# Performance work log

Hardware: AMD Instinct MI355X
Metric: run time of the kernel (lower is better)

Reference implementation:

```python
import jax, jax.numpy as jnp
import numpy as np

N, E = 50000, 600000
D_IN, D_H, D_OUT, D_E = 128, 128, 128, 32


def setup_inputs() -> dict:
    key = jax.random.key(0)
    ks = jax.random.split(key, 20)
    s = 0.05
    inp = {
        "x": jax.random.normal(ks[0], (N, D_IN), dtype=jnp.float32),
        "edge_index": jax.random.randint(ks[1], (2, E), 0, N, dtype=jnp.int64),
        "edge_attr": jax.random.normal(ks[2], (E, D_E), dtype=jnp.float32),
        # layer 0 (GINEConv MLP + edge lin: edge_dim -> in_channels)
        "w1_0": jax.random.normal(ks[3], (D_IN, D_H), dtype=jnp.float32) * s,
        "b1_0": jnp.zeros((D_H,), jnp.float32),
        "w2_0": jax.random.normal(ks[4], (D_H, D_H), dtype=jnp.float32) * s,
        "b2_0": jnp.zeros((D_H,), jnp.float32),
        "we_0": jax.random.normal(ks[5], (D_E, D_IN), dtype=jnp.float32) * s,
        "be_0": jnp.zeros((D_IN,), jnp.float32),
        # layer 1 (edge lin: edge_dim -> hidden_channels)
        "w1_1": jax.random.normal(ks[6], (D_H, D_H), dtype=jnp.float32) * s,
        "b1_1": jnp.zeros((D_H,), jnp.float32),
        "w2_1": jax.random.normal(ks[7], (D_H, D_H), dtype=jnp.float32) * s,
        "b2_1": jnp.zeros((D_H,), jnp.float32),
        "we_1": jax.random.normal(ks[8], (D_E, D_H), dtype=jnp.float32) * s,
        "be_1": jnp.zeros((D_H,), jnp.float32),
        # output head
        "fc1_w": jax.random.normal(ks[9], (D_H, D_H), dtype=jnp.float32) * s,
        "fc1_b": jnp.zeros((D_H,), jnp.float32),
        "fc2_w": jax.random.normal(ks[10], (D_H, D_OUT), dtype=jnp.float32) * s,
        "fc2_b": jnp.zeros((D_OUT,), jnp.float32),
    }
    return inp


def _gine_layer(x, src, dst, edge_attr, we, be, w1, b1, w2, b2):
    # GINEConv (eps=0): out = MLP(x + sum_j ReLU(x_j + edge_lin(e_ij)))
    e_emb = edge_attr @ we + be                       # [E, d]
    msg = jax.nn.relu(x[src] + e_emb)                 # gather + message
    agg = jax.ops.segment_sum(msg, dst, num_segments=x.shape[0])  # scatter-add
    h = agg + x                                       # (1 + eps) * x, eps = 0
    return jnp.maximum(h @ w1 + b1, 0.0) @ w2 + b2    # 2-layer MLP


def reference(x, edge_index, edge_attr,
              w1_0, b1_0, w2_0, b2_0, we_0, be_0,
              w1_1, b1_1, w2_1, b2_1, we_1, be_1,
              fc1_w, fc1_b, fc2_w, fc2_b):
    src, dst = edge_index[0], edge_index[1]
    h = _gine_layer(x, src, dst, edge_attr, we_0, be_0, w1_0, b1_0, w2_0, b2_0)
    h = jax.nn.relu(h)  # activation (dropout=0 -> identity)
    h = _gine_layer(h, src, dst, edge_attr, we_1, be_1, w1_1, b1_1, w2_1, b2_1)
    h = jax.nn.relu(h)
    h = jax.nn.relu(h @ fc1_w + fc1_b)
    return h @ fc2_w + fc2_b
```

## Files before the change

kernel.cpp:

```cpp
#include <hip/hip_runtime.h>
#include <stdint.h>


#define ND 128
#define ED 32

typedef __attribute__((ext_vector_type(8))) short short8;
typedef __attribute__((ext_vector_type(4))) float f32x4;

__device__ inline unsigned short bf16_hi(float f) {
    union { float f; unsigned u; } v;
    v.f = f;
    return (unsigned short)(v.u >> 16);
}
__device__ inline float bf16_f(unsigned short h) {
    union { unsigned u; float f; } v;
    v.u = ((unsigned)h) << 16;
    return v.f;
}

__global__ __launch_bounds__(256) void zero_kernel(int* __restrict__ p, int n) {
    int i = blockIdx.x * blockDim.x + threadIdx.x;
    if (i < n) p[i] = 0;
}

__global__ __launch_bounds__(256) void hist_kernel(const int* __restrict__ ei,
                                                   int* __restrict__ counts, int E) {
    int i = blockIdx.x * blockDim.x + threadIdx.x;
    if (i < E) atomicAdd(&counts[ei[E + i]], 1);
}

__global__ __launch_bounds__(256) void bsum_kernel(const int* __restrict__ counts,
                                                   int* __restrict__ bsum, int N) {
    __shared__ int s[256];
    int t = threadIdx.x;
    int i = blockIdx.x * 256 + t;
    s[t] = (i < N) ? counts[i] : 0;
    __syncthreads();
#pragma unroll
    for (int off = 128; off > 0; off >>= 1) {
        if (t < off) s[t] += s[t + off];
        __syncthreads();
    }
    if (t == 0) bsum[blockIdx.x] = s[0];
}

__global__ __launch_bounds__(256) void scan_bsums(const int* __restrict__ bsum,
                                                  int* __restrict__ bofs,
                                                  int* __restrict__ row_start_N, int NB) {
    __shared__ int s[256];
    int t = threadIdx.x;
    int chunk = (NB + 255) >> 8;
    int lo = min(t * chunk, NB);
    int hi = min(lo + chunk, NB);
    int sum = 0;
    for (int i = lo; i < hi; ++i) sum += bsum[i];
    s[t] = sum;
    __syncthreads();
    for (int off = 1; off < 256; off <<= 1) {
        int v = (t >= off) ? s[t - off] : 0;
        __syncthreads();
        s[t] += v;
        __syncthreads();
    }
    int pre = (t == 0) ? 0 : s[t - 1];
    for (int i = lo; i < hi; ++i) {
        bofs[i] = pre;
        pre += bsum[i];
    }
    if (t == 255) *row_start_N = s[255];
}

__global__ __launch_bounds__(256) void expand_kernel(const int* __restrict__ counts,
                                                     const int* __restrict__ bofs,
                                                     int* __restrict__ row_start,
                                                     int* __restrict__ woff, int N) {
    __shared__ int s[256];
    int t = threadIdx.x;
    int i = blockIdx.x * 256 + t;
    int c = (i < N) ? counts[i] : 0;
    s[t] = c;
    __syncthreads();
    for (int off = 1; off < 256; off <<= 1) {
        int v = (t >= off) ? s[t - off] : 0;
        __syncthreads();
        s[t] += v;
        __syncthreads();
    }
    if (i < N) {
        int pre = bofs[blockIdx.x] + s[t] - c;
        row_start[i] = pre;
        woff[i] = pre;
    }
}

__global__ __launch_bounds__(256) void scatter_kernel(const int* __restrict__ ei,
                                                      int* __restrict__ woff,
                                                      int2* __restrict__ pack, int E) {
    int i = blockIdx.x * blockDim.x + threadIdx.x;
    if (i < E) {
        int d = ei[E + i];
        int p = atomicAdd(&woff[d], 1);
        pack[p] = make_int2(ei[i], i);
    }
}

__global__ __launch_bounds__(256) void wrange_kernel(const int* __restrict__ row_start,
                                                     int* __restrict__ wstart,
                                                     int N, int E, int NW) {
    int w = blockIdx.x * 256 + threadIdx.x;
    if (w > NW) return;
    if (w == 0) { wstart[0] = 0; return; }
    if (w == NW) { wstart[NW] = N; return; }
    int T = (int)((long long)w * E / NW);
    int lo = 0, hi = N - 1;
    while (lo < hi) {
        int mid = (lo + hi) >> 1;
        if (row_start[mid + 1] > T) hi = mid; else lo = mid + 1;
    }
    wstart[w] = lo;
}

__global__ __launch_bounds__(256) void wprep_kernel(
    const float* __restrict__ w0, const float* __restrict__ w1,
    const float* __restrict__ w2, const float* __restrict__ w3,
    const float* __restrict__ w4, const float* __restrict__ w5,
    unsigned short* __restrict__ hi, unsigned short* __restrict__ lo) {
    int t = blockIdx.x * blockDim.x + threadIdx.x;
    const float* W;
    switch (blockIdx.y) {
        case 0: W = w0; break;
        case 1: W = w1; break;
        case 2: W = w2; break;
        case 3: W = w3; break;
        case 4: W = w4; break;
        default: W = w5; break;
    }
    unsigned short* dh = hi + (size_t)blockIdx.y * 16384;
    unsigned short* dl = lo + (size_t)blockIdx.y * 16384;
    int c = t >> 6, l = t & 63;
    int nt = c >> 2, ks = c & 3;
    int n = nt * 16 + (l & 15);
    int kb = ks * 32 + ((l >> 4) << 3);
#pragma unroll
    for (int j = 0; j < 8; ++j) {
        float f = W[(size_t)(kb + j) * ND + n];
        unsigned short h = bf16_hi(f);
        dh[((size_t)c * 64 + l) * 8 + j] = h;
        dl[((size_t)c * 64 + l) * 8 + j] = bf16_hi(f - bf16_f(h));
    }
}

__global__ __launch_bounds__(256) void wprep_we(const float* __restrict__ w0,
                                                const float* __restrict__ w1,
                                                unsigned short* __restrict__ hi) {
    int t = threadIdx.x;
    int c = (blockIdx.x << 2) + (t >> 6);
    int l = t & 63;
    const float* W = blockIdx.y ? w1 : w0;
    unsigned short* dh = hi + (size_t)blockIdx.y * 4096;
    int n = c * 16 + (l & 15);
    int kb = (l >> 4) << 3;
#pragma unroll
    for (int j = 0; j < 8; ++j)
        dh[((size_t)c * 64 + l) * 8 + j] = bf16_hi(W[(size_t)(kb + j) * ND + n]);
}

__global__ __launch_bounds__(256) void xprep_kernel(const float* __restrict__ X,
                                                    const float* __restrict__ be,
                                                    unsigned short* __restrict__ xpk,
                                                    int N) {
    int t = blockIdx.x * 256 + threadIdx.x;
    int total = (N + 1) * 16;
    if (t >= total) return;
    int v = t >> 4, g = t & 15;
    short8 h, l;
    if (v < N) {
        const float4* p = (const float4*)(X + (size_t)v * ND + g * 8);
        float4 a0 = p[0], a1 = p[1];
        float f[8] = {a0.x, a0.y, a0.z, a0.w, a1.x, a1.y, a1.z, a1.w};
#pragma unroll
        for (int j = 0; j < 8; ++j) {
            float fv = f[j] + be[g * 8 + j];
            unsigned short hh = bf16_hi(fv);
            h[j] = (short)hh;
            l[j] = (short)bf16_hi(fv - bf16_f(hh));
        }
    } else {
#pragma unroll
        for (int j = 0; j < 8; ++j) {
            h[j] = (short)0xC6EA;
            l[j] = 0;
        }
    }
    unsigned short* dst = xpk + (size_t)t * 16;
    *(short8*)dst = h;
    *(short8*)(dst + 8) = l;
}

__global__ __launch_bounds__(256, 4) void agg_mfma(
    const float* __restrict__ xin, const float* __restrict__ edge_attr,
    const unsigned short* __restrict__ xpk, const unsigned short* __restrict__ bfh,
    const int* __restrict__ row_start, const int* __restrict__ wstart,
    const int2* __restrict__ pack, float* __restrict__ hout, int N, int E) {
    int lane = threadIdx.x & 63;
    int gw = (blockIdx.x * blockDim.x + threadIdx.x) >> 6;
    int m = lane & 15;
    int quad = lane >> 4;

    short8 bh[8];
#pragma unroll
    for (int nt = 0; nt < 8; ++nt)
        bh[nt] = *(const short8*)(bfh + ((size_t)nt * 64 + lane) * 8);

    short8 idf[2];
#pragma unroll
    for (int q = 0; q < 2; ++q)
#pragma unroll
        for (int j = 0; j < 8; ++j)
            idf[q][j] = (quad * 8 + j == q * 16 + m) ? (short)0x3F80 : (short)0;

    int col0 = quad * 32 + m;
    int col1 = col0 + 16;

    int v_lo = wstart[gw];
    int v_hi = wstart[gw + 1];
    if (v_lo >= v_hi) return;

    int beg = row_start[v_lo];
    int2 pk2 = pack[min(beg + m, E - 1)];

    for (int v = v_lo; v < v_hi; ++v) {
        int end = row_start[v + 1];
        float res0 = xin[(size_t)v * ND + col0];
        float res1 = xin[(size_t)v * ND + col1];
        float part[8];
#pragma unroll
        for (int nt = 0; nt < 8; ++nt) part[nt] = 0.f;

        for (int base = beg; base < end; base += 16) {
            int2 pk = pk2;
            int nxt = (base + 16 < end) ? base + 16 : end;
            pk2 = pack[min(nxt + m, E - 1)];

            int rem = end - base;
            int s = (m < rem) ? pk.x : N;

            const unsigned short* xr = xpk + ((size_t)s * 16 + quad) * 16;
            short8 xh[4], xl[4];
#pragma unroll
            for (int kc = 0; kc < 4; ++kc) {
                xh[kc] = *(const short8*)(xr + kc * 64);
                xl[kc] = *(const short8*)(xr + kc * 64 + 8);
            }
            const float4* ar = (const float4*)(edge_attr + (size_t)pk.y * ED + quad * 8);
            float4 a0 = ar[0], a1 = ar[1];

            float af[8] = {a0.x, a0.y, a0.z, a0.w, a1.x, a1.y, a1.z, a1.w};
            short8 ah, al;
#pragma unroll
            for (int j = 0; j < 8; ++j) {
                unsigned short h = bf16_hi(af[j]);
                ah[j] = (short)h;
                al[j] = (short)bf16_hi(af[j] - bf16_f(h));
            }

#pragma unroll
            for (int nt = 0; nt < 8; ++nt) {
                f32x4 a = {0.f, 0.f, 0.f, 0.f};
                a = __builtin_amdgcn_mfma_f32_16x16x32_bf16(ah, bh[nt], a, 0, 0, 0);
                a = __builtin_amdgcn_mfma_f32_16x16x32_bf16(al, bh[nt], a, 0, 0, 0);
                a = __builtin_amdgcn_mfma_f32_16x16x32_bf16(xh[nt >> 1], idf[nt & 1], a,
                                                            0, 0, 0);
                a = __builtin_amdgcn_mfma_f32_16x16x32_bf16(xl[nt >> 1], idf[nt & 1], a,
                                                            0, 0, 0);
#pragma unroll
                for (int r = 0; r < 4; ++r)
                    part[nt] += fmaxf(a[r], 0.f);
            }
        }
#pragma unroll
        for (int nt = 0; nt < 8; ++nt) {
            float p = part[nt];
            p += __shfl_xor(p, 16, 64);
            p += __shfl_xor(p, 32, 64);
            part[nt] = p;
        }
        float o0 = quad == 0 ? part[0] : quad == 1 ? part[2] : quad == 2 ? part[4] : part[6];
        float o1 = quad == 0 ? part[1] : quad == 1 ? part[3] : quad == 2 ? part[5] : part[7];
        hout[(size_t)v * ND + col0] = res0 + o0;
        hout[(size_t)v * ND + col1] = res1 + o1;
        beg = end;
    }
}

#define LP 132
__global__ __launch_bounds__(256, 4) void mlp2_mfma(
    const float* __restrict__ A,
    const unsigned short* __restrict__ w1h, const unsigned short* __restrict__ w1l,
    const float* __restrict__ b1,
    const unsigned short* __restrict__ w2h, const unsigned short* __restrict__ w2l,
    const float* __restrict__ b2,
    float* __restrict__ C, int N, int relu2) {
    __shared__ float tile[4][16 * LP];
    int lane = threadIdx.x & 63;
    int wave = threadIdx.x >> 6;
    int gw = blockIdx.x * 4 + wave;
    int m0 = gw * 16;
    if (m0 >= N) return;
    int m = lane & 15;
    int quad = lane >> 4;
    float* T = tile[wave];

    int row = m0 + m;
    bool rok = row < N;
    short8 ah[4], al[4];
#pragma unroll
    for (int ks = 0; ks < 4; ++ks) {
        float f[8];
        if (rok) {
            const float4* p = (const float4*)(A + (size_t)row * ND + ks * 32 + quad * 8);
            float4 a0 = p[0], a1 = p[1];
            f[0] = a0.x; f[1] = a0.y; f[2] = a0.z; f[3] = a0.w;
            f[4] = a1.x; f[5] = a1.y; f[6] = a1.z; f[7] = a1.w;
        } else {
#pragma unroll
            for (int j = 0; j < 8; ++j) f[j] = 0.f;
        }
#pragma unroll
        for (int j = 0; j < 8; ++j) {
            unsigned short hh = bf16_hi(f[j]);
            ah[ks][j] = (short)hh;
            al[ks][j] = (short)bf16_hi(f[j] - bf16_f(hh));
        }
    }

#pragma unroll
    for (int nt = 0; nt < 8; ++nt) {
        f32x4 acc = {0.f, 0.f, 0.f, 0.f};
#pragma unroll
        for (int ks = 0; ks < 4; ++ks) {
            size_t off = ((size_t)(nt * 4 + ks) * 64 + lane) * 8;
            short8 bh = *(const short8*)(w1h + off);
            short8 bl = *(const short8*)(w1l + off);
            acc = __builtin_amdgcn_mfma_f32_16x16x32_bf16(ah[ks], bh, acc, 0, 0, 0);
            acc = __builtin_amdgcn_mfma_f32_16x16x32_bf16(al[ks], bh, acc, 0, 0, 0);
            acc = __builtin_amdgcn_mfma_f32_16x16x32_bf16(ah[ks], bl, acc, 0, 0, 0);
        }
        float bv = b1[nt * 16 + m];
#pragma unroll
        for (int r = 0; r < 4; ++r) {
            float o = acc[r] + bv;
            o = o > 0.f ? o : 0.f;
            T[(quad * 4 + r) * LP + nt * 16 + m] = o;
        }
    }

    short8 ch[4], cl[4];
#pragma unroll
    for (int ks = 0; ks < 4; ++ks) {
        const float4* p = (const float4*)(T + m * LP + ks * 32 + quad * 8);
        float4 a0 = p[0], a1 = p[1];
        float f[8] = {a0.x, a0.y, a0.z, a0.w, a1.x, a1.y, a1.z, a1.w};
#pragma unroll
        for (int j = 0; j < 8; ++j) {
            unsigned short hh = bf16_hi(f[j]);
            ch[ks][j] = (short)hh;
            cl[ks][j] = (short)bf16_hi(f[j] - bf16_f(hh));
        }
    }

#pragma unroll
    for (int nt = 0; nt < 8; ++nt) {
        f32x4 acc = {0.f, 0.f, 0.f, 0.f};
#pragma unroll
        for (int ks = 0; ks < 4; ++ks) {
            size_t off = ((size_t)(nt * 4 + ks) * 64 + lane) * 8;
            short8 bh = *(const short8*)(w2h + off);
            short8 bl = *(const short8*)(w2l + off);
            acc = __builtin_amdgcn_mfma_f32_16x16x32_bf16(ch[ks], bh, acc, 0, 0, 0);
            acc = __builtin_amdgcn_mfma_f32_16x16x32_bf16(cl[ks], bh, acc, 0, 0, 0);
            acc = __builtin_amdgcn_mfma_f32_16x16x32_bf16(ch[ks], bl, acc, 0, 0, 0);
        }
        float bv = b2[nt * 16 + m];
#pragma unroll
        for (int r = 0; r < 4; ++r) {
            int rr = m0 + quad * 4 + r;
            if (rr < N) {
                float o = acc[r] + bv;
                if (relu2) o = o > 0.f ? o : 0.f;
                C[(size_t)rr * ND + nt * 16 + m] = o;
            }
        }
    }
}

extern "C" void kernel_launch(void* const* d_in, const int* in_sizes, int n_in,
                              void* d_out, int out_size, void* d_ws, size_t ws_size,
                              hipStream_t stream) {
    const float* x = (const float*)d_in[0];
    const int* ei = (const int*)d_in[1];
    const float* ea = (const float*)d_in[2];
    const float* w1_0 = (const float*)d_in[3];
    const float* b1_0 = (const float*)d_in[4];
    const float* w2_0 = (const float*)d_in[5];
    const float* b2_0 = (const float*)d_in[6];
    const float* we_0 = (const float*)d_in[7];
    const float* be_0 = (const float*)d_in[8];
    const float* w1_1 = (const float*)d_in[9];
    const float* b1_1 = (const float*)d_in[10];
    const float* w2_1 = (const float*)d_in[11];
    const float* b2_1 = (const float*)d_in[12];
    const float* we_1 = (const float*)d_in[13];
    const float* be_1 = (const float*)d_in[14];
    const float* fc1_w = (const float*)d_in[15];
    const float* fc1_b = (const float*)d_in[16];
    const float* fc2_w = (const float*)d_in[17];
    const float* fc2_b = (const float*)d_in[18];

    int N = in_sizes[0] / ND;
    int E = in_sizes[2] / ED;
    int NB = (N + 255) / 256;
    const int NW = 4096;

    float* bufA = (float*)d_ws;
    int* counts = (int*)(bufA + (size_t)N * ND);
    int* row_start = counts + N;
    int* woff = row_start + (N + 1);
    int* bsum = woff + N;
    int* bofs = bsum + NB;
    int* wstart = bofs + NB;
    int2* pack = (int2*)((((uintptr_t)(wstart + NW + 1)) + 15) & ~(uintptr_t)15);
    unsigned short* wfh = (unsigned short*)(pack + E);
    unsigned short* wfl = wfh + 6 * 16384;
    unsigned short* weh = wfl + 6 * 16384;
    unsigned short* xpk = weh + 2 * 4096;
    float* out = (float*)d_out;

    zero_kernel<<<(N + 255) / 256, 256, 0, stream>>>(counts, N);
    hist_kernel<<<(E + 255) / 256, 256, 0, stream>>>(ei, counts, E);
    bsum_kernel<<<NB, 256, 0, stream>>>(counts, bsum, N);
    scan_bsums<<<1, 256, 0, stream>>>(bsum, bofs, row_start + N, NB);
    expand_kernel<<<NB, 256, 0, stream>>>(counts, bofs, row_start, woff, N);
    scatter_kernel<<<(E + 255) / 256, 256, 0, stream>>>(ei, woff, pack, E);
    wrange_kernel<<<(NW + 1 + 255) / 256, 256, 0, stream>>>(row_start, wstart, N, E, NW);
    wprep_kernel<<<dim3(8, 6), 256, 0, stream>>>(w1_0, w2_0, w1_1, w2_1, fc1_w, fc2_w,
                                                 wfh, wfl);
    wprep_we<<<dim3(2, 2), 256, 0, stream>>>(we_0, we_1, weh);

    int gg = ((N + 15) / 16 + 3) / 4;
    int gx = ((N + 1) * 16 + 255) / 256;

    xprep_kernel<<<gx, 256, 0, stream>>>(x, be_0, xpk, N);
    agg_mfma<<<NW / 4, 256, 0, stream>>>(x, ea, xpk, weh, row_start, wstart, pack, out,
                                         N, E);
    mlp2_mfma<<<gg, 256, 0, stream>>>(out, wfh + 0 * 16384, wfl + 0 * 16384, b1_0,
                                      wfh + 1 * 16384, wfl + 1 * 16384, b2_0, bufA, N, 1);

    xprep_kernel<<<gx, 256, 0, stream>>>(bufA, be_1, xpk, N);
    agg_mfma<<<NW / 4, 256, 0, stream>>>(bufA, ea, xpk, weh + 4096, row_start, wstart,
                                         pack, out, N, E);
    mlp2_mfma<<<gg, 256, 0, stream>>>(out, wfh + 2 * 16384, wfl + 2 * 16384, b1_1,
                                      wfh + 3 * 16384, wfl + 3 * 16384, b2_1, bufA, N, 1);

    mlp2_mfma<<<gg, 256, 0, stream>>>(bufA, wfh + 4 * 16384, wfl + 4 * 16384, fc1_b,
                                      wfh + 5 * 16384, wfl + 5 * 16384, fc2_b, out, N, 0);
}
```

Before: 492.3 us.

## Merge prep kernels into fewer launches and fuse layer-1 x packing into MLP epilogue

Folds the counts zeroing, the weight split/pack, the edge-weight pack and the layer-0 x packing into a single block-indexed prep kernel, and merges the CSR scatter with the warp-range search. The layer-1 x packing (adding be_1 and splitting into bf16 hi/lo) now runs in the epilogue of the first MLP kernel from its shared-memory tile, instead of a separate pass that reloads the activations from global memory. This cuts kernel launches and one full read of the hidden activations. In exchange the fused epilogue does not write the padding row N, and the MLP kernel carries extra register and branch cost.

```diff
diff --git a/kernel.cpp b/kernel.cpp
--- a/kernel.cpp
+++ b/kernel.cpp
@@ -17,11 +17,6 @@
     union { unsigned u; float f; } v;
     v.u = ((unsigned)h) << 16;
     return v.f;
-}
-
-__global__ __launch_bounds__(256) void zero_kernel(int* __restrict__ p, int n) {
-    int i = blockIdx.x * blockDim.x + threadIdx.x;
-    if (i < n) p[i] = 0;
 }
 
 __global__ __launch_bounds__(256) void hist_kernel(const int* __restrict__ ei,
@@ -94,21 +89,22 @@
     }
 }
 
-__global__ __launch_bounds__(256) void scatter_kernel(const int* __restrict__ ei,
-                                                      int* __restrict__ woff,
-                                                      int2* __restrict__ pack, int E) {
-    int i = blockIdx.x * blockDim.x + threadIdx.x;
-    if (i < E) {
-        int d = ei[E + i];
-        int p = atomicAdd(&woff[d], 1);
-        pack[p] = make_int2(ei[i], i);
-    }
-}
-
-__global__ __launch_bounds__(256) void wrange_kernel(const int* __restrict__ row_start,
-                                                     int* __restrict__ wstart,
-                                                     int N, int E, int NW) {
-    int w = blockIdx.x * 256 + threadIdx.x;
+__global__ __launch_bounds__(256) void scatter_wrange(
+    const int* __restrict__ ei, int* __restrict__ woff, int2* __restrict__ pack,
+    int E, const int* __restrict__ row_start, int* __restrict__ wstart,
+    int N, int NW) {
+    int b = blockIdx.x;
+    int SB = (E + 255) >> 8;
+    if (b < SB) {
+        int i = b * 256 + threadIdx.x;
+        if (i < E) {
+            int d = ei[E + i];
+            int p = atomicAdd(&woff[d], 1);
+            pack[p] = make_int2(ei[i], i);
+        }
+        return;
+    }
+    int w = (b - SB) * 256 + threadIdx.x;
     if (w > NW) return;
     if (w == 0) { wstart[0] = 0; return; }
     if (w == NW) { wstart[NW] = N; return; }
@@ -121,56 +117,67 @@
     wstart[w] = lo;
 }
 
-__global__ __launch_bounds__(256) void wprep_kernel(
+__global__ __launch_bounds__(256) void prepwx_kernel(
+    int* __restrict__ counts, int N,
     const float* __restrict__ w0, const float* __restrict__ w1,
     const float* __restrict__ w2, const float* __restrict__ w3,
     const float* __restrict__ w4, const float* __restrict__ w5,
-    unsigned short* __restrict__ hi, unsigned short* __restrict__ lo) {
-    int t = blockIdx.x * blockDim.x + threadIdx.x;
-    const float* W;
-    switch (blockIdx.y) {
-        case 0: W = w0; break;
-        case 1: W = w1; break;
-        case 2: W = w2; break;
-        case 3: W = w3; break;
-        case 4: W = w4; break;
-        default: W = w5; break;
-    }
-    unsigned short* dh = hi + (size_t)blockIdx.y * 16384;
-    unsigned short* dl = lo + (size_t)blockIdx.y * 16384;
-    int c = t >> 6, l = t & 63;
-    int nt = c >> 2, ks = c & 3;
-    int n = nt * 16 + (l & 15);
-    int kb = ks * 32 + ((l >> 4) << 3);
-#pragma unroll
-    for (int j = 0; j < 8; ++j) {
-        float f = W[(size_t)(kb + j) * ND + n];
-        unsigned short h = bf16_hi(f);
-        dh[((size_t)c * 64 + l) * 8 + j] = h;
-        dl[((size_t)c * 64 + l) * 8 + j] = bf16_hi(f - bf16_f(h));
-    }
-}
-
-__global__ __launch_bounds__(256) void wprep_we(const float* __restrict__ w0,
-                                                const float* __restrict__ w1,
-                                                unsigned short* __restrict__ hi) {
-    int t = threadIdx.x;
-    int c = (blockIdx.x << 2) + (t >> 6);
-    int l = t & 63;
-    const float* W = blockIdx.y ? w1 : w0;
-    unsigned short* dh = hi + (size_t)blockIdx.y * 4096;
-    int n = c * 16 + (l & 15);
-    int kb = (l >> 4) << 3;
-#pragma unroll
-    for (int j = 0; j < 8; ++j)
-        dh[((size_t)c * 64 + l) * 8 + j] = bf16_hi(W[(size_t)(kb + j) * ND + n]);
-}
-
-__global__ __launch_bounds__(256) void xprep_kernel(const float* __restrict__ X,
-                                                    const float* __restrict__ be,
-                                                    unsigned short* __restrict__ xpk,
-                                                    int N) {
-    int t = blockIdx.x * 256 + threadIdx.x;
+    unsigned short* __restrict__ hi, unsigned short* __restrict__ lo,
+    const float* __restrict__ e0, const float* __restrict__ e1,
+    unsigned short* __restrict__ weh,
+    const float* __restrict__ X, const float* __restrict__ be,
+    unsigned short* __restrict__ xpk) {
+    int b = blockIdx.x;
+    int ZB = (N + 255) >> 8;
+    if (b < ZB) {
+        int i = b * 256 + threadIdx.x;
+        if (i < N) counts[i] = 0;
+        return;
+    }
+    b -= ZB;
+    if (b < 48) {
+        int y = b >> 3;
+        int t = (b & 7) * 256 + threadIdx.x;
+        const float* W;
+        switch (y) {
+            case 0: W = w0; break;
+            case 1: W = w1; break;
+            case 2: W = w2; break;
+            case 3: W = w3; break;
+            case 4: W = w4; break;
+            default: W = w5; break;
+        }
+        unsigned short* dh = hi + (size_t)y * 16384;
+        unsigned short* dl = lo + (size_t)y * 16384;
+        int c = t >> 6, l = t & 63;
+        int nt = c >> 2, ks = c & 3;
+        int n = nt * 16 + (l & 15);
+        int kb = ks * 32 + ((l >> 4) << 3);
+#pragma unroll
+        for (int j = 0; j < 8; ++j) {
+            float f = W[(size_t)(kb + j) * ND + n];
+            unsigned short h = bf16_hi(f);
+            dh[((size_t)c * 64 + l) * 8 + j] = h;
+            dl[((size_t)c * 64 + l) * 8 + j] = bf16_hi(f - bf16_f(h));
+        }
+        return;
+    }
+    b -= 48;
+    if (b < 4) {
+        int t = threadIdx.x;
+        int c = ((b & 1) << 2) + (t >> 6);
+        int l = t & 63;
+        const float* W = (b >> 1) ? e1 : e0;
+        unsigned short* dh = weh + (size_t)(b >> 1) * 4096;
+        int n = c * 16 + (l & 15);
+        int kb = (l >> 4) << 3;
+#pragma unroll
+        for (int j = 0; j < 8; ++j)
+            dh[((size_t)c * 64 + l) * 8 + j] = bf16_hi(W[(size_t)(kb + j) * ND + n]);
+        return;
+    }
+    b -= 4;
+    int t = b * 256 + threadIdx.x;
     int total = (N + 1) * 16;
     if (t >= total) return;
     int v = t >> 4, g = t & 15;
@@ -301,7 +308,8 @@
     const float* __restrict__ b1,
     const unsigned short* __restrict__ w2h, const unsigned short* __restrict__ w2l,
     const float* __restrict__ b2,
-    float* __restrict__ C, int N, int relu2) {
+    float* __restrict__ C, int N, int relu2,
+    const float* __restrict__ ben, unsigned short* __restrict__ xpk) {
     __shared__ float tile[4][16 * LP];
     int lane = threadIdx.x & 63;
     int wave = threadIdx.x >> 6;
@@ -386,10 +394,35 @@
 #pragma unroll
         for (int r = 0; r < 4; ++r) {
             int rr = m0 + quad * 4 + r;
+            float o = acc[r] + bv;
+            if (relu2) o = o > 0.f ? o : 0.f;
+            if (rr < N) C[(size_t)rr * ND + nt * 16 + m] = o;
+            if (xpk) T[(quad * 4 + r) * LP + nt * 16 + m] = o;
+        }
+    }
+
+    if (xpk) {
+#pragma unroll
+        for (int i = 0; i < 4; ++i) {
+            int task = lane + 64 * i;
+            int rl = task >> 4;
+            int g = task & 15;
+            int rr = m0 + rl;
             if (rr < N) {
-                float o = acc[r] + bv;
-                if (relu2) o = o > 0.f ? o : 0.f;
-                C[(size_t)rr * ND + nt * 16 + m] = o;
+                const float4* p = (const float4*)(T + rl * LP + g * 8);
+                float4 a0 = p[0], a1 = p[1];
+                float f[8] = {a0.x, a0.y, a0.z, a0.w, a1.x, a1.y, a1.z, a1.w};
+                short8 h, l;
+#pragma unroll
+                for (int j = 0; j < 8; ++j) {
+                    float fv = f[j] + ben[g * 8 + j];
+                    unsigned short hh = bf16_hi(fv);
+                    h[j] = (short)hh;
+                    l[j] = (short)bf16_hi(fv - bf16_f(hh));
+                }
+                unsigned short* dst = xpk + ((size_t)rr * 16 + g) * 16;
+                *(short8*)dst = h;
+                *(short8*)(dst + 8) = l;
             }
         }
     }
@@ -437,32 +470,35 @@
     unsigned short* xpk = weh + 2 * 4096;
     float* out = (float*)d_out;
 
-    zero_kernel<<<(N + 255) / 256, 256, 0, stream>>>(counts, N);
+    int ZB = (N + 255) / 256;
+    int gx = ((N + 1) * 16 + 255) / 256;
+    int SB = (E + 255) / 256;
+    int WB = (NW + 1 + 255) / 256;
+    int gg = ((N + 15) / 16 + 3) / 4;
+
+    prepwx_kernel<<<ZB + 48 + 4 + gx, 256, 0, stream>>>(
+        counts, N, w1_0, w2_0, w1_1, w2_1, fc1_w, fc2_w, wfh, wfl,
+        we_0, we_1, weh, x, be_0, xpk);
     hist_kernel<<<(E + 255) / 256, 256, 0, stream>>>(ei, counts, E);
     bsum_kernel<<<NB, 256, 0, stream>>>(counts, bsum, N);
     scan_bsums<<<1, 256, 0, stream>>>(bsum, bofs, row_start + N, NB);
     expand_kernel<<<NB, 256, 0, stream>>>(counts, bofs, row_start, woff, N);
-    scatter_kernel<<<(E + 255) / 256, 256, 0, stream>>>(ei, woff, pack, E);
-    wrange_kernel<<<(NW + 1 + 255) / 256, 256, 0, stream>>>(row_start, wstart, N, E, NW);
-    wprep_kernel<<<dim3(8, 6), 256, 0, stream>>>(w1_0, w2_0, w1_1, w2_1, fc1_w, fc2_w,
-                                                 wfh, wfl);
-    wprep_we<<<dim3(2, 2), 256, 0, stream>>>(we_0, we_1, weh);
-
-    int gg = ((N + 15) / 16 + 3) / 4;
-    int gx = ((N + 1) * 16 + 255) / 256;
-
-    xprep_kernel<<<gx, 256, 0, stream>>>(x, be_0, xpk, N);
+    scatter_wrange<<<SB + WB, 256, 0, stream>>>(ei, woff, pack, E, row_start, wstart,
+                                                N, NW);
+
     agg_mfma<<<NW / 4, 256, 0, stream>>>(x, ea, xpk, weh, row_start, wstart, pack, out,
                                          N, E);
     mlp2_mfma<<<gg, 256, 0, stream>>>(out, wfh + 0 * 16384, wfl + 0 * 16384, b1_0,
-                                      wfh + 1 * 16384, wfl + 1 * 16384, b2_0, bufA, N, 1);
-
-    xprep_kernel<<<gx, 256, 0, stream>>>(bufA, be_1, xpk, N);
+                                      wfh + 1 * 16384, wfl + 1 * 16384, b2_0, bufA, N, 1,
+                                      be_1, xpk);
+
     agg_mfma<<<NW / 4, 256, 0, stream>>>(bufA, ea, xpk, weh + 4096, row_start, wstart,
                                          pack, out, N, E);
     mlp2_mfma<<<gg, 256, 0, stream>>>(out, wfh + 2 * 16384, wfl + 2 * 16384, b1_1,
-                                      wfh + 3 * 16384, wfl + 3 * 16384, b2_1, bufA, N, 1);
+                                      wfh + 3 * 16384, wfl + 3 * 16384, b2_1, bufA, N, 1,
+                                      nullptr, nullptr);
 
     mlp2_mfma<<<gg, 256, 0, stream>>>(bufA, wfh + 4 * 16384, wfl + 4 * 16384, fc1_b,
-                                      wfh + 5 * 16384, wfl + 5 * 16384, fc2_b, out, N, 0);
-}
+                                      wfh + 5 * 16384, wfl + 5 * 16384, fc2_b, out, N, 0,
+                                      nullptr, nullptr);
+}
```

Result: faster. 470.5 us (-4.4%).
